# Kernel optimization log

Hardware: AMD Instinct MI355X
Metric: run time of the kernel (lower is better)

## Reference

```python
import jax, jax.numpy as jnp
import numpy as np

N_NODES = 100000
N_EDGES = 3200000
N_GRAPHS = 256
IN_CH = 8
HID = 64


def _gcn_conv(x, W, b, src, dst, n):
    # PyG GCNConv default: add self-loops, symmetric normalization.
    # out_i = sum_{j->i} d_i^-1/2 d_j^-1/2 (xW)_j + (1/d_i)(xW)_i + b
    xw = x @ W                                     # [N, out]
    deg = jax.ops.segment_sum(jnp.ones_like(dst, dtype=xw.dtype), dst,
                              num_segments=n) + 1.0  # +1 for self-loop
    dinv = jax.lax.rsqrt(deg)
    norm = dinv[src] * dinv[dst]                   # [E]
    agg = jax.ops.segment_sum(xw[src] * norm[:, None], dst, num_segments=n)
    agg = agg + xw * (1.0 / deg)[:, None]          # self-loop term (norm = 1/deg)
    return agg + b


def setup_inputs() -> dict:
    key = jax.random.key(0)
    ks = jax.random.split(key, 12)
    x = jax.random.normal(ks[0], (N_NODES, IN_CH), dtype=jnp.float32)
    edge_index = jax.random.randint(ks[1], (2, N_EDGES), 0, N_NODES, dtype=jnp.int64)
    batch = jnp.sort(jax.random.randint(ks[2], (N_NODES,), 0, N_GRAPHS, dtype=jnp.int64))

    def glorot(k, fan_in, fan_out):
        s = jnp.sqrt(2.0 / (fan_in + fan_out)).astype(jnp.float32)
        return jax.random.normal(k, (fan_in, fan_out), dtype=jnp.float32) * s

    return {
        "x": x, "edge_index": edge_index, "batch": batch,
        "W1": glorot(ks[3], IN_CH, HID), "b1": jnp.zeros((HID,), jnp.float32),
        "W2": glorot(ks[4], HID, 2 * HID), "b2": jnp.zeros((2 * HID,), jnp.float32),
        "W3": glorot(ks[5], 2 * HID, HID), "b3": jnp.zeros((HID,), jnp.float32),
        "Wl1": glorot(ks[6], HID, HID // 2), "bl1": jnp.zeros((HID // 2,), jnp.float32),
        "Wl2": glorot(ks[7], HID // 2, 1), "bl2": jnp.zeros((1,), jnp.float32),
    }


def reference(x, edge_index, batch, W1, b1, W2, b2, W3, b3, Wl1, bl1, Wl2, bl2):
    src, dst = edge_index[0], edge_index[1]
    h = jax.nn.relu(_gcn_conv(x, W1, b1, src, dst, N_NODES))
    h = jax.nn.relu(_gcn_conv(h, W2, b2, src, dst, N_NODES))
    h = jax.nn.relu(_gcn_conv(h, W3, b3, src, dst, N_NODES))
    # global mean pool over graphs
    sums = jax.ops.segment_sum(h, batch, num_segments=N_GRAPHS)
    cnts = jax.ops.segment_sum(jnp.ones((N_NODES,), h.dtype), batch, num_segments=N_GRAPHS)
    g = sums / jnp.maximum(cnts, 1.0)[:, None]     # [G, HID]
    g = jax.nn.relu(g @ Wl1 + bl1)
    out = g @ Wl2 + bl2                            # [G, 1]
    return out[:, 0]
```

## Files before the change

kernel.cpp:

```cpp
#include <hip/hip_runtime.h>
#include <hip/hip_bf16.h>

#define N_NODES 100000
#define N_EDGES 3200000
#define N_GRAPHS 256
#define NB_BUCKETS 196
#define BSHIFT 9
#define NBLK 256
#define SCAN_BLKS 49
#define CSR_CAP 22528

#define OFF_SUMS      0u
#define OFF_CNTF      65536u
#define ZERO_BYTES    66560u
#define OFF_HIST      66560u
#define OFF_BSUM      267264u
#define OFF_ROWPTR    267776u
#define OFF_DINV      668160u
#define OFF_COL       1068544u
#define OFF_XS1       13868544u
#define OFF_BUFQ      20268544u
#define OFF_BUFR      45868544u
#define OFF_BUFP      71468544u
#define OFF_PAIRS     OFF_BUFP

typedef __attribute__((ext_vector_type(8))) short bf16x8;
typedef __attribute__((ext_vector_type(4))) float f32x4;

__device__ __forceinline__ unsigned short f2bf(float f) {
    unsigned u = __float_as_uint(f);
    return (unsigned short)((u + 0x7fffu + ((u >> 16) & 1u)) >> 16);
}

__device__ __forceinline__ float bf2f(unsigned short h) {
    return __uint_as_float(((unsigned)h) << 16);
}

__device__ __forceinline__ void acc_bf8(uint4 v, float m, float* a) {
    a[0] += m * __uint_as_float(v.x << 16);
    a[1] += m * __uint_as_float(v.x & 0xffff0000u);
    a[2] += m * __uint_as_float(v.y << 16);
    a[3] += m * __uint_as_float(v.y & 0xffff0000u);
    a[4] += m * __uint_as_float(v.z << 16);
    a[5] += m * __uint_as_float(v.z & 0xffff0000u);
    a[6] += m * __uint_as_float(v.w << 16);
    a[7] += m * __uint_as_float(v.w & 0xffff0000u);
}

__global__ __launch_bounds__(256) void hist_kernel(const int* __restrict__ dst,
                                                   int* __restrict__ hist,
                                                   int* __restrict__ zbase,
                                                   int E, int epb) {
    __shared__ int h[NB_BUCKETS];
    int t = threadIdx.x, blk = blockIdx.x;
    int gid = blk * 256 + t;
    if (gid < (int)(ZERO_BYTES / 4)) zbase[gid] = 0;
    if (t < NB_BUCKETS) h[t] = 0;
    __syncthreads();
    int e0 = blk * epb, e1 = min(e0 + epb, E);
    for (int e = e0 + t; e < e1; e += 256)
        atomicAdd(&h[__builtin_nontemporal_load(&dst[e]) >> BSHIFT], 1);
    __syncthreads();
    if (t < NB_BUCKETS) hist[t * NBLK + blk] = h[t];
}

__global__ __launch_bounds__(1024) void scanhA_kernel(int* __restrict__ hist,
                                                      int* __restrict__ bsum) {
    __shared__ int s[1024];
    int t = threadIdx.x;
    int i = blockIdx.x * 1024 + t;
    int v = hist[i];
    s[t] = v;
    __syncthreads();
    for (int off = 1; off < 1024; off <<= 1) {
        int add = (t >= off) ? s[t - off] : 0;
        __syncthreads();
        s[t] += add;
        __syncthreads();
    }
    hist[i] = s[t] - v;
    if (t == 1023) bsum[blockIdx.x] = s[t];
}

__global__ __launch_bounds__(256) void bin_kernel(const int* __restrict__ src,
                                                  const int* __restrict__ dst,
                                                  const int* __restrict__ hist,
                                                  const int* __restrict__ bsum,
                                                  int* __restrict__ packed, int E, int epb) {
    __shared__ int cur[NB_BUCKETS];
    __shared__ int boffL[SCAN_BLKS];
    int t = threadIdx.x, blk = blockIdx.x;
    if (t < 64) {
        int orig = (t < SCAN_BLKS) ? bsum[t] : 0;
        int v = orig;
        for (int off = 1; off < 64; off <<= 1) {
            int up = __shfl_up(v, off);
            if (t >= off) v += up;
        }
        if (t < SCAN_BLKS) boffL[t] = v - orig;
    }
    __syncthreads();
    if (t < NB_BUCKETS) {
        int i = t * NBLK + blk;
        cur[t] = hist[i] + boffL[i >> 10];
    }
    __syncthreads();
    int e0 = blk * epb, e1 = min(e0 + epb, E);
    for (int e = e0 + t; e < e1; e += 256) {
        int d = __builtin_nontemporal_load(&dst[e]);
        int sv = __builtin_nontemporal_load(&src[e]);
        int pos = atomicAdd(&cur[d >> BSHIFT], 1);
        packed[pos] = ((d & 511) << 17) | sv;
    }
}

__global__ __launch_bounds__(512) void csr_kernel(const int* __restrict__ packed,
                                                  const int* __restrict__ hist,
                                                  const int* __restrict__ bsum,
                                                  const float* __restrict__ x,
                                                  int* __restrict__ row_ptr,
                                                  float* __restrict__ dinv,
                                                  unsigned short* __restrict__ xs1,
                                                  int* __restrict__ col, int E) {
    __shared__ int cntL[512];
    __shared__ int rsL[512];
    __shared__ int fillL[512];
    __shared__ int boffL[SCAN_BLKS];
    __shared__ int srcL[CSR_CAP];
    int t = threadIdx.x, b = blockIdx.x;
    int lo = b << BSHIFT;
    int nloc = min(512, N_NODES - lo);
    cntL[t] = 0;
    fillL[t] = 0;
    if (t < 64) {
        int orig = (t < SCAN_BLKS) ? bsum[t] : 0;
        int v = orig;
        for (int off = 1; off < 64; off <<= 1) {
            int up = __shfl_up(v, off);
            if (t >= off) v += up;
        }
        if (t < SCAN_BLKS) boffL[t] = v - orig;
    }
    __syncthreads();
    int i0 = b * NBLK;
    int start = hist[i0] + boffL[i0 >> 10];
    int end;
    if (b == NB_BUCKETS - 1) end = E;
    else {
        int i1 = (b + 1) * NBLK;
        end = hist[i1] + boffL[i1 >> 10];
    }
    for (int e = start + t; e < end; e += 512)
        atomicAdd(&cntL[packed[e] >> 17], 1);
    __syncthreads();
    int v = cntL[t];
    __syncthreads();
    for (int off = 1; off < 512; off <<= 1) {
        int add = (t >= off) ? cntL[t - off] : 0;
        __syncthreads();
        cntL[t] += add;
        __syncthreads();
    }
    int rowstart = start + cntL[t] - v;
    rsL[t] = rowstart;
    if (t < nloc) {
        int node = lo + t;
        row_ptr[node] = rowstart;
        float d = rsqrtf((float)(v + 1));
        dinv[node] = d;
        const float4* xv = reinterpret_cast<const float4*>(x) + node * 2;
        float4 xa = xv[0], xb = xv[1];
        uint4 p;
        p.x = (unsigned)f2bf(xa.x * d) | ((unsigned)f2bf(xa.y * d) << 16);
        p.y = (unsigned)f2bf(xa.z * d) | ((unsigned)f2bf(xa.w * d) << 16);
        p.z = (unsigned)f2bf(xb.x * d) | ((unsigned)f2bf(xb.y * d) << 16);
        p.w = (unsigned)f2bf(xb.z * d) | ((unsigned)f2bf(xb.w * d) << 16);
        *reinterpret_cast<uint4*>(&xs1[node * 8]) = p;
    }
    if (b == NB_BUCKETS - 1 && t == 0) row_ptr[N_NODES] = E;
    __syncthreads();
    for (int e = start + t; e < end; e += 512) {
        int p = packed[e];
        int dl = p >> 17;
        int pos = rsL[dl] + atomicAdd(&fillL[dl], 1);
        int rel = pos - start;
        if (rel < CSR_CAP) srcL[rel] = p & 0x1FFFF;
        else col[pos] = p & 0x1FFFF;
    }
    __syncthreads();
    int lim = min(end - start, CSR_CAP);
    for (int i = t; i < lim; i += 512)
        col[start + i] = srcL[i];
}

__global__ __launch_bounds__(256) void agg8g1_kernel(
        const unsigned short* __restrict__ xs, const int* __restrict__ row_ptr,
        const int* __restrict__ col, const float* __restrict__ dinv,
        const float* __restrict__ W1, const float* __restrict__ b1,
        unsigned short* __restrict__ xs2, int n) {
    int wave = threadIdx.x >> 6;
    int node = blockIdx.x * 4 + wave;
    if (node >= n) return;
    int lane = threadIdx.x & 63;
    int f = lane & 7;
    int s = lane >> 3;
    float w[8];
    float bias = b1[lane];
#pragma unroll
    for (int k = 0; k < 8; ++k) w[k] = W1[k * 64 + lane];
    int e0 = row_ptr[node], e1 = row_ptr[node + 1];
    float a = (s == 0) ? bf2f(xs[node * 8 + f]) : 0.0f;
    int base = e0;
    for (; e1 - base > 48; base += 48) {
#pragma unroll
        for (int g = 0; g < 6; ++g) {
            int c = __builtin_nontemporal_load(&col[base + 8 * g + s]);
            a += bf2f(xs[c * 8 + f]);
        }
    }
    int rem = e1 - base;
    if (rem > 0) {
        int e1m1 = e1 - 1;
        bool g4 = rem > 32, g5 = rem > 40;
        int i0 = base + s,      i1 = base + 8 + s,  i2 = base + 16 + s;
        int i3 = base + 24 + s, i4 = base + 32 + s, i5 = base + 40 + s;
        int c0 = __builtin_nontemporal_load(&col[min(i0, e1m1)]);
        int c1 = __builtin_nontemporal_load(&col[min(i1, e1m1)]);
        int c2 = __builtin_nontemporal_load(&col[min(i2, e1m1)]);
        int c3 = __builtin_nontemporal_load(&col[min(i3, e1m1)]);
        int c4 = 0, c5 = 0;
        if (g4) c4 = __builtin_nontemporal_load(&col[min(i4, e1m1)]);
        if (g5) c5 = __builtin_nontemporal_load(&col[min(i5, e1m1)]);
        float v0 = bf2f(xs[c0 * 8 + f]);
        float v1 = bf2f(xs[c1 * 8 + f]);
        float v2 = bf2f(xs[c2 * 8 + f]);
        float v3 = bf2f(xs[c3 * 8 + f]);
        float v4 = 0.f, v5 = 0.f;
        if (g4) v4 = bf2f(xs[c4 * 8 + f]);
        if (g5) v5 = bf2f(xs[c5 * 8 + f]);
        a += ((i0 < e1) ? v0 : 0.f) + ((i1 < e1) ? v1 : 0.f);
        a += ((i2 < e1) ? v2 : 0.f) + ((i3 < e1) ? v3 : 0.f);
        if (g4) a += (i4 < e1) ? v4 : 0.f;
        if (g5) a += (i5 < e1) ? v5 : 0.f;
    }
    a += __shfl_xor(a, 8);
    a += __shfl_xor(a, 16);
    a += __shfl_xor(a, 32);
    float d = dinv[node];
    float zd = a * d;
    float acc = bias;
#pragma unroll
    for (int k = 0; k < 8; ++k) acc += __shfl(zd, k) * w[k];
    xs2[node * 64 + lane] = f2bf(d * fmaxf(acc, 0.0f));
}

__global__ __launch_bounds__(256) void agg64bf_kernel(
        const unsigned short* __restrict__ xs, const int* __restrict__ row_ptr,
        const int* __restrict__ col, const float* __restrict__ dinv,
        unsigned short* __restrict__ z, int n) {
    int wave = threadIdx.x >> 6;
    int node = blockIdx.x * 4 + wave;
    if (node >= n) return;
    int lane = threadIdx.x & 63;
    int j = lane >> 3, l = lane & 7;
    int e0 = row_ptr[node], e1 = row_ptr[node + 1];
    float a[8] = {0.f, 0.f, 0.f, 0.f, 0.f, 0.f, 0.f, 0.f};
    uint4 sv = *reinterpret_cast<const uint4*>(&xs[node * 64 + 8 * l]);
    int base = e0;
    for (; e1 - base > 48; base += 32) {
        int s0 = __builtin_nontemporal_load(&col[base + j]);
        int s1 = __builtin_nontemporal_load(&col[base + 8 + j]);
        int s2 = __builtin_nontemporal_load(&col[base + 16 + j]);
        int s3 = __builtin_nontemporal_load(&col[base + 24 + j]);
        uint4 v0 = *reinterpret_cast<const uint4*>(&xs[s0 * 64 + 8 * l]);
        uint4 v1 = *reinterpret_cast<const uint4*>(&xs[s1 * 64 + 8 * l]);
        uint4 v2 = *reinterpret_cast<const uint4*>(&xs[s2 * 64 + 8 * l]);
        uint4 v3 = *reinterpret_cast<const uint4*>(&xs[s3 * 64 + 8 * l]);
        acc_bf8(v0, 1.f, a); acc_bf8(v1, 1.f, a);
        acc_bf8(v2, 1.f, a); acc_bf8(v3, 1.f, a);
    }
    int rem = e1 - base;
    if (rem > 0) {
        int e1m1 = e1 - 1;
        bool g4 = rem > 32, g5 = rem > 40;
        int i0 = base + j,      i1 = base + 8 + j;
        int i2 = base + 16 + j, i3 = base + 24 + j;
        int i4 = base + 32 + j, i5 = base + 40 + j;
        int c0 = __builtin_nontemporal_load(&col[min(i0, e1m1)]);
        int c1 = __builtin_nontemporal_load(&col[min(i1, e1m1)]);
        int c2 = __builtin_nontemporal_load(&col[min(i2, e1m1)]);
        int c3 = __builtin_nontemporal_load(&col[min(i3, e1m1)]);
        int c4 = 0, c5 = 0;
        if (g4) c4 = __builtin_nontemporal_load(&col[min(i4, e1m1)]);
        if (g5) c5 = __builtin_nontemporal_load(&col[min(i5, e1m1)]);
        uint4 v0 = *reinterpret_cast<const uint4*>(&xs[c0 * 64 + 8 * l]);
        uint4 v1 = *reinterpret_cast<const uint4*>(&xs[c1 * 64 + 8 * l]);
        uint4 v2 = *reinterpret_cast<const uint4*>(&xs[c2 * 64 + 8 * l]);
        uint4 v3 = *reinterpret_cast<const uint4*>(&xs[c3 * 64 + 8 * l]);
        uint4 v4, v5;
        if (g4) v4 = *reinterpret_cast<const uint4*>(&xs[c4 * 64 + 8 * l]);
        if (g5) v5 = *reinterpret_cast<const uint4*>(&xs[c5 * 64 + 8 * l]);
        acc_bf8(v0, (i0 < e1) ? 1.f : 0.f, a);
        acc_bf8(v1, (i1 < e1) ? 1.f : 0.f, a);
        acc_bf8(v2, (i2 < e1) ? 1.f : 0.f, a);
        acc_bf8(v3, (i3 < e1) ? 1.f : 0.f, a);
        if (g4) acc_bf8(v4, (i4 < e1) ? 1.f : 0.f, a);
        if (g5) acc_bf8(v5, (i5 < e1) ? 1.f : 0.f, a);
    }
    acc_bf8(sv, (j == 0) ? 1.f : 0.f, a);
#pragma unroll
    for (int k = 0; k < 8; ++k) {
        a[k] += __shfl_xor(a[k], 8);
        a[k] += __shfl_xor(a[k], 16);
        a[k] += __shfl_xor(a[k], 32);
    }
    if (j == 0) {
        float d = dinv[node];
        uint4 p;
        p.x = (unsigned)f2bf(a[0] * d) | ((unsigned)f2bf(a[1] * d) << 16);
        p.y = (unsigned)f2bf(a[2] * d) | ((unsigned)f2bf(a[3] * d) << 16);
        p.z = (unsigned)f2bf(a[4] * d) | ((unsigned)f2bf(a[5] * d) << 16);
        p.w = (unsigned)f2bf(a[6] * d) | ((unsigned)f2bf(a[7] * d) << 16);
        *reinterpret_cast<uint4*>(&z[node * 64 + 8 * l]) = p;
    }
}

__global__ __launch_bounds__(256) void mgemm23_kernel(
        const unsigned short* __restrict__ X,
        const float* __restrict__ W2, const float* __restrict__ b2,
        const float* __restrict__ W3, const float* __restrict__ dinv,
        unsigned short* __restrict__ Y,
        int nrows) {
    __shared__ unsigned short Wt2[128 * 72];
    __shared__ unsigned short Wt3[64 * 136];
    __shared__ unsigned short h2L[64 * 136];
    int tid = threadIdx.x;
    for (int i = tid; i < 64 * 128; i += 256) {
        int k = i / 128, m = i % 128;
        Wt2[m * 72 + k] = f2bf(W2[i]);
    }
    for (int i = tid; i < 128 * 64; i += 256) {
        int k = i / 64, m = i % 64;
        Wt3[m * 136 + k] = f2bf(W3[i]);
    }
    __syncthreads();
    int wave = tid >> 6, lane = tid & 63;
    int row0 = blockIdx.x * 64 + wave * 16;
    int hl = lane >> 4, ll = lane & 15;
    int arow = min(row0 + ll, nrows - 1);
    bf16x8 af0 = *reinterpret_cast<const bf16x8*>(&X[arow * 64 + hl * 8]);
    bf16x8 af1 = *reinterpret_cast<const bf16x8*>(&X[arow * 64 + 32 + hl * 8]);
    f32x4 acc1[8];
#pragma unroll
    for (int nt = 0; nt < 8; ++nt) {
        float bv = b2[nt * 16 + ll];
        acc1[nt] = {bv, bv, bv, bv};
    }
#pragma unroll
    for (int nt = 0; nt < 8; ++nt) {
        bf16x8 b0 = *reinterpret_cast<const bf16x8*>(&Wt2[(nt * 16 + ll) * 72 + hl * 8]);
        bf16x8 b1 = *reinterpret_cast<const bf16x8*>(&Wt2[(nt * 16 + ll) * 72 + 32 + hl * 8]);
        acc1[nt] = __builtin_amdgcn_mfma_f32_16x16x32_bf16(af0, b0, acc1[nt], 0, 0, 0);
        acc1[nt] = __builtin_amdgcn_mfma_f32_16x16x32_bf16(af1, b1, acc1[nt], 0, 0, 0);
    }
#pragma unroll
    for (int nt = 0; nt < 8; ++nt) {
#pragma unroll
        for (int r = 0; r < 4; ++r) {
            float v = fmaxf(acc1[nt][r], 0.0f);
            h2L[(wave * 16 + hl * 4 + r) * 136 + nt * 16 + ll] = f2bf(v);
        }
    }
    __syncthreads();
    bf16x8 af2[4];
#pragma unroll
    for (int ks = 0; ks < 4; ++ks)
        af2[ks] = *reinterpret_cast<const bf16x8*>(
            &h2L[(wave * 16 + ll) * 136 + ks * 32 + hl * 8]);
    f32x4 acc2[4];
#pragma unroll
    for (int nt = 0; nt < 4; ++nt) acc2[nt] = {0.f, 0.f, 0.f, 0.f};
#pragma unroll
    for (int nt = 0; nt < 4; ++nt) {
#pragma unroll
        for (int ks = 0; ks < 4; ++ks) {
            bf16x8 bf = *reinterpret_cast<const bf16x8*>(
                &Wt3[(nt * 16 + ll) * 136 + ks * 32 + hl * 8]);
            acc2[nt] = __builtin_amdgcn_mfma_f32_16x16x32_bf16(af2[ks], bf, acc2[nt], 0, 0, 0);
        }
    }
#pragma unroll
    for (int r = 0; r < 4; ++r) {
        int row = row0 + hl * 4 + r;
        if (row < nrows) {
            float d = dinv[row];
#pragma unroll
            for (int nt = 0; nt < 4; ++nt)
                Y[row * 64 + nt * 16 + ll] = f2bf(acc2[nt][r] * d);
        }
    }
}

#define POOL_NPB 128
__global__ __launch_bounds__(256) void pool_kernel(
        const unsigned short* __restrict__ z3, const float* __restrict__ b3,
        const int* __restrict__ batch, float* __restrict__ sums,
        float* __restrict__ cntf, int n) {
    int wave = threadIdx.x >> 6;
    int lane = threadIdx.x & 63;
    int node0 = blockIdx.x * POOL_NPB + wave * 32;
    int nodeEnd = min(node0 + 32, n);
    if (node0 >= n) return;
    float bias = b3[lane];
    float acc = 0.0f, cnt = 0.0f;
    int curg = -1;
    for (int node = node0; node < nodeEnd; ++node) {
        int g = batch[node];
        if (g != curg) {
            if (curg >= 0) {
                atomicAdd(&sums[curg * 64 + lane], acc);
                if (lane == 0) atomicAdd(&cntf[curg], cnt);
            }
            curg = g; acc = 0.0f; cnt = 0.0f;
        }
        acc += fmaxf(bf2f(z3[node * 64 + lane]) + bias, 0.0f);
        cnt += 1.0f;
    }
    if (curg >= 0) {
        atomicAdd(&sums[curg * 64 + lane], acc);
        if (lane == 0) atomicAdd(&cntf[curg], cnt);
    }
}

__global__ void mlp_kernel(const float* __restrict__ sums, const float* __restrict__ cntf,
                           const float* __restrict__ Wl1, const float* __restrict__ bl1,
                           const float* __restrict__ Wl2, const float* __restrict__ bl2,
                           float* __restrict__ out) {
    __shared__ float gv[64];
    __shared__ float hid[32];
    int g = blockIdx.x, t = threadIdx.x;
    float denom = fmaxf(cntf[g], 1.0f);
    gv[t] = sums[g * 64 + t] / denom;
    __syncthreads();
    if (t < 32) {
        float a = bl1[t];
#pragma unroll
        for (int k = 0; k < 64; ++k) a += gv[k] * Wl1[k * 32 + t];
        hid[t] = fmaxf(a, 0.0f);
    }
    __syncthreads();
    if (t == 0) {
        float o = bl2[0];
#pragma unroll
        for (int k = 0; k < 32; ++k) o += hid[k] * Wl2[k];
        out[g] = o;
    }
}

extern "C" void kernel_launch(void* const* d_in, const int* in_sizes, int n_in,
                              void* d_out, int out_size, void* d_ws, size_t ws_size,
                              hipStream_t stream) {
    const float* x   = (const float*)d_in[0];
    const int* ei    = (const int*)d_in[1];
    const int* batch = (const int*)d_in[2];
    const float* W1  = (const float*)d_in[3];
    const float* b1  = (const float*)d_in[4];
    const float* W2  = (const float*)d_in[5];
    const float* b2  = (const float*)d_in[6];
    const float* W3  = (const float*)d_in[7];
    const float* b3  = (const float*)d_in[8];
    const float* Wl1 = (const float*)d_in[9];
    const float* bl1 = (const float*)d_in[10];
    const float* Wl2 = (const float*)d_in[11];
    const float* bl2 = (const float*)d_in[12];
    float* out = (float*)d_out;

    const int N = N_NODES;
    const int E = in_sizes[1] / 2;
    const int* src = ei;
    const int* dst = ei + E;

    char* ws = (char*)d_ws;
    float* sums    = (float*)(ws + OFF_SUMS);
    float* cntf    = (float*)(ws + OFF_CNTF);
    int*   hist    = (int*)(ws + OFF_HIST);
    int*   bsum    = (int*)(ws + OFF_BSUM);
    int*   row_ptr = (int*)(ws + OFF_ROWPTR);
    float* dinv    = (float*)(ws + OFF_DINV);
    int*   col     = (int*)(ws + OFF_COL);
    unsigned short* xs1 = (unsigned short*)(ws + OFF_XS1);
    unsigned short* bufQ = (unsigned short*)(ws + OFF_BUFQ);
    unsigned short* bufR = (unsigned short*)(ws + OFF_BUFR);
    int*   packed  = (int*)(ws + OFF_PAIRS);

    int epb = (E + NBLK - 1) / NBLK;
    hist_kernel<<<NBLK, 256, 0, stream>>>(dst, hist, (int*)ws, E, epb);
    scanhA_kernel<<<SCAN_BLKS, 1024, 0, stream>>>(hist, bsum);
    bin_kernel<<<NBLK, 256, 0, stream>>>(src, dst, hist, bsum, packed, E, epb);
    csr_kernel<<<NB_BUCKETS, 512, 0, stream>>>(packed, hist, bsum, x,
                                               row_ptr, dinv, xs1, col, E);

    agg8g1_kernel<<<(N + 3) / 4, 256, 0, stream>>>(xs1, row_ptr, col, dinv, W1, b1,
                                                   bufQ, N);

    agg64bf_kernel<<<(N + 3) / 4, 256, 0, stream>>>(
        bufQ, row_ptr, col, dinv, bufR, N);

    mgemm23_kernel<<<1563, 256, 0, stream>>>(bufR, W2, b2, W3, dinv, bufQ, N);

    agg64bf_kernel<<<(N + 3) / 4, 256, 0, stream>>>(
        bufQ, row_ptr, col, dinv, bufR, N);

    pool_kernel<<<(N + POOL_NPB - 1) / POOL_NPB, 256, 0, stream>>>(
        bufR, b3, batch, sums, cntf, N);
    mlp_kernel<<<N_GRAPHS, 64, 0, stream>>>(sums, cntf, Wl1, bl1, Wl2, bl2, out);
}
```

Measured before the change: 355.5 us.

## Precompute bf16 transposed weights once and split aggregation launches into node chunks

The W2/W3 transpose and bf16 conversion moves out of every mgemm23 block and into the scan kernel, done once into workspace. Each mgemm23 block then copies the prepared weights into shared memory with vector loads. Each 64-channel aggregation is also split into three launches over node ranges, likely so each launch's destination-node writes and its share of the gather stay more cache-resident. The split adds launch overhead and tail gaps between launches.

```diff
diff --git a/kernel.cpp b/kernel.cpp
--- a/kernel.cpp
+++ b/kernel.cpp
@@ -19,10 +19,14 @@
 #define OFF_DINV      668160u
 #define OFF_COL       1068544u
 #define OFF_XS1       13868544u
+#define OFF_WPRE      15468544u
 #define OFF_BUFQ      20268544u
 #define OFF_BUFR      45868544u
 #define OFF_BUFP      71468544u
 #define OFF_PAIRS     OFF_BUFP
+
+#define WPRE_W3OFF 9216
+#define WPRE_TOT   17920
 
 typedef __attribute__((ext_vector_type(8))) short bf16x8;
 typedef __attribute__((ext_vector_type(4))) float f32x4;
@@ -65,10 +69,21 @@
 }
 
 __global__ __launch_bounds__(1024) void scanhA_kernel(int* __restrict__ hist,
-                                                      int* __restrict__ bsum) {
+                                                      int* __restrict__ bsum,
+                                                      const float* __restrict__ W2,
+                                                      const float* __restrict__ W3,
+                                                      unsigned short* __restrict__ wpre) {
     __shared__ int s[1024];
     int t = threadIdx.x;
     int i = blockIdx.x * 1024 + t;
+    if (i < 8192) {
+        int m = i >> 6, k = i & 63;
+        wpre[m * 72 + k] = f2bf(W2[k * 128 + m]);
+    } else if (i < 16384) {
+        int ii = i - 8192;
+        int m = ii >> 7, k = ii & 127;
+        wpre[WPRE_W3OFF + m * 136 + k] = f2bf(W3[k * 64 + m]);
+    }
     int v = hist[i];
     s[t] = v;
     __syncthreads();
@@ -257,10 +272,10 @@
 __global__ __launch_bounds__(256) void agg64bf_kernel(
         const unsigned short* __restrict__ xs, const int* __restrict__ row_ptr,
         const int* __restrict__ col, const float* __restrict__ dinv,
-        unsigned short* __restrict__ z, int n) {
+        unsigned short* __restrict__ z, int n0, int n1) {
     int wave = threadIdx.x >> 6;
-    int node = blockIdx.x * 4 + wave;
-    if (node >= n) return;
+    int node = n0 + blockIdx.x * 4 + wave;
+    if (node >= n1) return;
     int lane = threadIdx.x & 63;
     int j = lane >> 3, l = lane & 7;
     int e0 = row_ptr[node], e1 = row_ptr[node + 1];
@@ -327,21 +342,17 @@
 
 __global__ __launch_bounds__(256) void mgemm23_kernel(
         const unsigned short* __restrict__ X,
-        const float* __restrict__ W2, const float* __restrict__ b2,
-        const float* __restrict__ W3, const float* __restrict__ dinv,
+        const unsigned short* __restrict__ wpre,
+        const float* __restrict__ b2, const float* __restrict__ dinv,
         unsigned short* __restrict__ Y,
         int nrows) {
-    __shared__ unsigned short Wt2[128 * 72];
-    __shared__ unsigned short Wt3[64 * 136];
+    __shared__ __align__(16) unsigned short WtL[WPRE_TOT];
     __shared__ unsigned short h2L[64 * 136];
     int tid = threadIdx.x;
-    for (int i = tid; i < 64 * 128; i += 256) {
-        int k = i / 128, m = i % 128;
-        Wt2[m * 72 + k] = f2bf(W2[i]);
-    }
-    for (int i = tid; i < 128 * 64; i += 256) {
-        int k = i / 64, m = i % 64;
-        Wt3[m * 136 + k] = f2bf(W3[i]);
+    {
+        const uint4* src4 = reinterpret_cast<const uint4*>(wpre);
+        uint4* dst4 = reinterpret_cast<uint4*>(WtL);
+        for (int i = tid; i < WPRE_TOT / 8; i += 256) dst4[i] = src4[i];
     }
     __syncthreads();
     int wave = tid >> 6, lane = tid & 63;
@@ -358,8 +369,8 @@
     }
 #pragma unroll
     for (int nt = 0; nt < 8; ++nt) {
-        bf16x8 b0 = *reinterpret_cast<const bf16x8*>(&Wt2[(nt * 16 + ll) * 72 + hl * 8]);
-        bf16x8 b1 = *reinterpret_cast<const bf16x8*>(&Wt2[(nt * 16 + ll) * 72 + 32 + hl * 8]);
+        bf16x8 b0 = *reinterpret_cast<const bf16x8*>(&WtL[(nt * 16 + ll) * 72 + hl * 8]);
+        bf16x8 b1 = *reinterpret_cast<const bf16x8*>(&WtL[(nt * 16 + ll) * 72 + 32 + hl * 8]);
         acc1[nt] = __builtin_amdgcn_mfma_f32_16x16x32_bf16(af0, b0, acc1[nt], 0, 0, 0);
         acc1[nt] = __builtin_amdgcn_mfma_f32_16x16x32_bf16(af1, b1, acc1[nt], 0, 0, 0);
     }
@@ -385,7 +396,7 @@
 #pragma unroll
         for (int ks = 0; ks < 4; ++ks) {
             bf16x8 bf = *reinterpret_cast<const bf16x8*>(
-                &Wt3[(nt * 16 + ll) * 136 + ks * 32 + hl * 8]);
+                &WtL[WPRE_W3OFF + (nt * 16 + ll) * 136 + ks * 32 + hl * 8]);
             acc2[nt] = __builtin_amdgcn_mfma_f32_16x16x32_bf16(af2[ks], bf, acc2[nt], 0, 0, 0);
         }
     }
@@ -488,14 +499,15 @@
     int*   row_ptr = (int*)(ws + OFF_ROWPTR);
     float* dinv    = (float*)(ws + OFF_DINV);
     int*   col     = (int*)(ws + OFF_COL);
-    unsigned short* xs1 = (unsigned short*)(ws + OFF_XS1);
+    unsigned short* xs1  = (unsigned short*)(ws + OFF_XS1);
+    unsigned short* wpre = (unsigned short*)(ws + OFF_WPRE);
     unsigned short* bufQ = (unsigned short*)(ws + OFF_BUFQ);
     unsigned short* bufR = (unsigned short*)(ws + OFF_BUFR);
     int*   packed  = (int*)(ws + OFF_PAIRS);
 
     int epb = (E + NBLK - 1) / NBLK;
     hist_kernel<<<NBLK, 256, 0, stream>>>(dst, hist, (int*)ws, E, epb);
-    scanhA_kernel<<<SCAN_BLKS, 1024, 0, stream>>>(hist, bsum);
+    scanhA_kernel<<<SCAN_BLKS, 1024, 0, stream>>>(hist, bsum, W2, W3, wpre);
     bin_kernel<<<NBLK, 256, 0, stream>>>(src, dst, hist, bsum, packed, E, epb);
     csr_kernel<<<NB_BUCKETS, 512, 0, stream>>>(packed, hist, bsum, x,
                                                row_ptr, dinv, xs1, col, E);
@@ -503,13 +515,20 @@
     agg8g1_kernel<<<(N + 3) / 4, 256, 0, stream>>>(xs1, row_ptr, col, dinv, W1, b1,
                                                    bufQ, N);
 
-    agg64bf_kernel<<<(N + 3) / 4, 256, 0, stream>>>(
-        bufQ, row_ptr, col, dinv, bufR, N);
-
-    mgemm23_kernel<<<1563, 256, 0, stream>>>(bufR, W2, b2, W3, dinv, bufQ, N);
-
-    agg64bf_kernel<<<(N + 3) / 4, 256, 0, stream>>>(
-        bufQ, row_ptr, col, dinv, bufR, N);
+    const int T = 33334;
+    for (int q = 0; q < 3; ++q) {
+        int n0 = q * T, n1 = min(n0 + T, N);
+        agg64bf_kernel<<<(n1 - n0 + 3) / 4, 256, 0, stream>>>(
+            bufQ, row_ptr, col, dinv, bufR, n0, n1);
+    }
+
+    mgemm23_kernel<<<1563, 256, 0, stream>>>(bufR, wpre, b2, dinv, bufQ, N);
+
+    for (int q = 0; q < 3; ++q) {
+        int n0 = q * T, n1 = min(n0 + T, N);
+        agg64bf_kernel<<<(n1 - n0 + 3) / 4, 256, 0, stream>>>(
+            bufQ, row_ptr, col, dinv, bufR, n0, n1);
+    }
 
     pool_kernel<<<(N + POOL_NPB - 1) / POOL_NPB, 256, 0, stream>>>(
         bufR, b3, batch, sums, cntf, N);
```

Result: slower. 366.6 us (+3.1%).
